# Performance work log

Measured on AMD Instinct MI355X. Metric: run time of the kernel, lower is better.

The kernel has to match this reference:

```python
import jax, jax.numpy as jnp
import numpy as np

B, T, L, D = 4, 64, 4096, 4096
MASK_VALUE = -1000000000.0


def setup_inputs() -> dict:
    key = jax.random.key(0)
    kq, km, ka = jax.random.split(key, 3)
    Q = jax.random.normal(kq, (1, T, D), dtype=jnp.float32)          # learned queries
    mask = jax.random.normal(km, (B, L, D), dtype=jnp.float32)       # acts as K and V
    attn_mask = jax.random.randint(ka, (B, T, L), 0, 2).astype(bool)  # True -> masked
    return {"mask": mask, "Q": Q, "attn_mask": attn_mask}


def reference(mask, Q, attn_mask):
    # scores: [B, T, L] = Q @ mask^T / sqrt(D)   (Q broadcast over batch)
    scale = 1.0 / np.sqrt(D).astype(np.float32)
    scores = jnp.einsum('td,bld->btl', Q[0], mask) * scale
    scores = jnp.where(attn_mask, MASK_VALUE, scores)
    attn = jax.nn.softmax(scores, axis=-1)
    # context: [B, T, D] = attn @ mask
    context = jnp.einsum('btl,bld->btd', attn, mask)
    return context
```

## Files before the change

### kernel.cpp

```cpp
#include <hip/hip_runtime.h>
#include <hip/hip_bf16.h>
#include <stdint.h>

#define B_ 4
#define T_ 64
#define L_ 4096
#define D_ 4096

using bf8   = __attribute__((ext_vector_type(8))) short;
using f32x4 = __attribute__((ext_vector_type(4))) float;

__device__ __forceinline__ unsigned short f2bf(float f) {
    union { float f; unsigned int u; } v;
    v.f = f;
    unsigned int r = v.u + 0x7fffu + ((v.u >> 16) & 1u);
    return (unsigned short)(r >> 16);
}

__device__ __forceinline__ int swz16(int row, int byteoff) {
    return byteoff ^ (((row ^ (row >> 3)) & 7) << 4);
}

__device__ __forceinline__ bf8 read_frag(const unsigned short* lds, int row, int kk, int lane) {
    int byte = kk * 64 + ((lane >> 4) << 4);
    int off  = row * 128 + swz16(row, byte);
    return *reinterpret_cast<const bf8*>(reinterpret_cast<const char*>(lds) + off);
}

__global__ __launch_bounds__(256, 2) void k_scores(
    const float* __restrict__ mask, const float* __restrict__ Q,
    float* __restrict__ scores) {
    __shared__ unsigned short lA[2][64 * 64];
    __shared__ unsigned short lB[2][32 * 64];
    const int tid  = threadIdx.x;
    const int lane = tid & 63;
    const int wave = tid >> 6;
    const int wm = wave >> 1, wn = wave & 1;
    const int b  = blockIdx.y;
    const int l0 = blockIdx.x * 32;
    const float* __restrict__ Mb = mask + (size_t)b * L_ * D_;

    f32x4 acc[2] = {};
    float4 ra[4], rb[2];

    auto loadTiles = [&](int k0) {
#pragma unroll
        for (int s = 0; s < 4; ++s) {
            int slot = tid + s * 256;
            int r = slot >> 4, c4 = slot & 15;
            ra[s] = *(reinterpret_cast<const float4*>(Q + (size_t)r * D_ + k0) + c4);
        }
#pragma unroll
        for (int s = 0; s < 2; ++s) {
            int slot = tid + s * 256;
            int r = slot >> 4, c4 = slot & 15;
            rb[s] = *(reinterpret_cast<const float4*>(Mb + (size_t)(l0 + r) * D_ + k0) + c4);
        }
    };
    auto writeTiles = [&](int buf) {
#pragma unroll
        for (int s = 0; s < 4; ++s) {
            int slot = tid + s * 256;
            int r = slot >> 4, c4 = slot & 15;
            int off = r * 128 + swz16(r, c4 * 8);
            ushort4 ua;
            ua.x = f2bf(ra[s].x); ua.y = f2bf(ra[s].y); ua.z = f2bf(ra[s].z); ua.w = f2bf(ra[s].w);
            *reinterpret_cast<ushort4*>(reinterpret_cast<char*>(lA[buf]) + off) = ua;
        }
#pragma unroll
        for (int s = 0; s < 2; ++s) {
            int slot = tid + s * 256;
            int r = slot >> 4, c4 = slot & 15;
            int off = r * 128 + swz16(r, c4 * 8);
            ushort4 ub;
            ub.x = f2bf(rb[s].x); ub.y = f2bf(rb[s].y); ub.z = f2bf(rb[s].z); ub.w = f2bf(rb[s].w);
            *reinterpret_cast<ushort4*>(reinterpret_cast<char*>(lB[buf]) + off) = ub;
        }
    };

    loadTiles(0);
    writeTiles(0);
    __syncthreads();
    const int NT = D_ / 64;
    for (int kt = 0; kt < NT; ++kt) {
        int cur = kt & 1;
        if (kt + 1 < NT) loadTiles((kt + 1) * 64);
#pragma unroll
        for (int kk = 0; kk < 2; ++kk) {
            bf8 a0 = read_frag(lA[cur], wm * 32 +      (lane & 15), kk, lane);
            bf8 a1 = read_frag(lA[cur], wm * 32 + 16 + (lane & 15), kk, lane);
            bf8 b0 = read_frag(lB[cur], wn * 16 +      (lane & 15), kk, lane);
            acc[0] = __builtin_amdgcn_mfma_f32_16x16x32_bf16(a0, b0, acc[0], 0, 0, 0);
            acc[1] = __builtin_amdgcn_mfma_f32_16x16x32_bf16(a1, b0, acc[1], 0, 0, 0);
        }
        if (kt + 1 < NT) writeTiles(cur ^ 1);
        __syncthreads();
    }

    const int rgrp = (lane >> 4) * 4;
    const int cidx = lane & 15;
#pragma unroll
    for (int mi = 0; mi < 2; ++mi)
#pragma unroll
        for (int r = 0; r < 4; ++r) {
            int t = wm * 32 + mi * 16 + rgrp + r;
            int l = l0 + wn * 16 + cidx;
            scores[((size_t)b * T_ + t) * L_ + l] = acc[mi][r] * 0.015625f;
        }
}

__global__ __launch_bounds__(256, 4) void k_softmax(
    const float* __restrict__ scores, const int* __restrict__ am,
    unsigned short* __restrict__ attn) {
    const int row  = blockIdx.x;
    const int tid  = threadIdx.x;
    const int lane = tid & 63;
    const int wave = tid >> 6;
    const float* __restrict__ s = scores + (size_t)row * L_;
    const int*   __restrict__ m = am     + (size_t)row * L_;
    __shared__ float redmax[4], redsum[4];

    float v[16];
#pragma unroll
    for (int j = 0; j < 4; ++j) {
        float4 f = *(reinterpret_cast<const float4*>(s) + tid + j * 256);
        int4   q = *(reinterpret_cast<const int4*>(m)   + tid + j * 256);
        v[j * 4 + 0] = q.x ? -1.0e9f : f.x;
        v[j * 4 + 1] = q.y ? -1.0e9f : f.y;
        v[j * 4 + 2] = q.z ? -1.0e9f : f.z;
        v[j * 4 + 3] = q.w ? -1.0e9f : f.w;
    }
    float mx = -3.0e38f;
#pragma unroll
    for (int i = 0; i < 16; ++i) mx = fmaxf(mx, v[i]);
#pragma unroll
    for (int off = 32; off; off >>= 1) mx = fmaxf(mx, __shfl_xor(mx, off, 64));
    if (lane == 0) redmax[wave] = mx;
    __syncthreads();
    mx = fmaxf(fmaxf(redmax[0], redmax[1]), fmaxf(redmax[2], redmax[3]));

    float z = 0.f;
#pragma unroll
    for (int i = 0; i < 16; ++i) {
        v[i] = exp2f((v[i] - mx) * 1.4426950408889634f);
        z += v[i];
    }
#pragma unroll
    for (int off = 32; off; off >>= 1) z += __shfl_xor(z, off, 64);
    if (lane == 0) redsum[wave] = z;
    __syncthreads();
    z = (redsum[0] + redsum[1]) + (redsum[2] + redsum[3]);
    float inv = 1.0f / z;

    unsigned short* __restrict__ arow = attn + (size_t)row * L_;
#pragma unroll
    for (int j = 0; j < 4; ++j) {
        ushort4 u;
        u.x = f2bf(v[j * 4 + 0] * inv);
        u.y = f2bf(v[j * 4 + 1] * inv);
        u.z = f2bf(v[j * 4 + 2] * inv);
        u.w = f2bf(v[j * 4 + 3] * inv);
        *(reinterpret_cast<ushort4*>(arow) + tid + j * 256) = u;
    }
}

__global__ __launch_bounds__(256, 2) void k_context(
    const float* __restrict__ mask, const unsigned short* __restrict__ attn,
    float* __restrict__ out) {
    __shared__ unsigned short lA[2][64 * 64];
    __shared__ unsigned short lB[2][32 * 64];
    const int tid  = threadIdx.x;
    const int lane = tid & 63;
    const int wave = tid >> 6;
    const int wm = wave >> 1, wn = wave & 1;
    const int b  = blockIdx.y;
    const int d0 = blockIdx.x * 32;
    const float*          __restrict__ Mb = mask + (size_t)b * L_ * D_;
    const unsigned short* __restrict__ Ab = attn + (size_t)b * T_ * L_;

    f32x4 acc[2] = {};
    uint4  raA[2];
    float4 rbB[2];

    auto loadTiles = [&](int k0) {
#pragma unroll
        for (int s = 0; s < 2; ++s) {
            int slot = tid + s * 256;
            int r = slot >> 3, c8 = slot & 7;
            raA[s] = *(reinterpret_cast<const uint4*>(Ab + (size_t)r * L_ + k0) + c8);
        }
#pragma unroll
        for (int s = 0; s < 2; ++s) {
            int slot = tid + s * 256;
            int kl = slot >> 3, d4 = slot & 7;
            rbB[s] = *(reinterpret_cast<const float4*>(Mb + (size_t)(k0 + kl) * D_ + d0) + d4);
        }
    };
    auto writeTiles = [&](int buf) {
#pragma unroll
        for (int s = 0; s < 2; ++s) {
            int slot = tid + s * 256;
            int r = slot >> 3, c8 = slot & 7;
            int off = r * 128 + swz16(r, c8 * 16);
            *reinterpret_cast<uint4*>(reinterpret_cast<char*>(lA[buf]) + off) = raA[s];
        }
#pragma unroll
        for (int s = 0; s < 2; ++s) {
            int slot = tid + s * 256;
            int kl = slot >> 3, d4 = slot & 7;
            float fv[4] = { rbB[s].x, rbB[s].y, rbB[s].z, rbB[s].w };
#pragma unroll
            for (int i = 0; i < 4; ++i) {
                int d = d4 * 4 + i;
                int off = d * 128 + swz16(d, kl * 2);
                *reinterpret_cast<unsigned short*>(reinterpret_cast<char*>(lB[buf]) + off) = f2bf(fv[i]);
            }
        }
    };

    loadTiles(0);
    writeTiles(0);
    __syncthreads();
    const int NT = L_ / 64;
    for (int kt = 0; kt < NT; ++kt) {
        int cur = kt & 1;
        if (kt + 1 < NT) loadTiles((kt + 1) * 64);
#pragma unroll
        for (int kk = 0; kk < 2; ++kk) {
            bf8 a0 = read_frag(lA[cur], wm * 32 +      (lane & 15), kk, lane);
            bf8 a1 = read_frag(lA[cur], wm * 32 + 16 + (lane & 15), kk, lane);
            bf8 b0 = read_frag(lB[cur], wn * 16 +      (lane & 15), kk, lane);
            acc[0] = __builtin_amdgcn_mfma_f32_16x16x32_bf16(a0, b0, acc[0], 0, 0, 0);
            acc[1] = __builtin_amdgcn_mfma_f32_16x16x32_bf16(a1, b0, acc[1], 0, 0, 0);
        }
        if (kt + 1 < NT) writeTiles(cur ^ 1);
        __syncthreads();
    }

    const int rgrp = (lane >> 4) * 4;
    const int cidx = lane & 15;
#pragma unroll
    for (int mi = 0; mi < 2; ++mi)
#pragma unroll
        for (int r = 0; r < 4; ++r) {
            int t = wm * 32 + mi * 16 + rgrp + r;
            int d = d0 + wn * 16 + cidx;
            out[((size_t)b * T_ + t) * D_ + d] = acc[mi][r];
        }
}

extern "C" void kernel_launch(void* const* d_in, const int* in_sizes, int n_in,
                              void* d_out, int out_size, void* d_ws, size_t ws_size,
                              hipStream_t stream) {
    const float* mask = (const float*)d_in[0];
    const float* Q    = (const float*)d_in[1];
    const int*   am   = (const int*)d_in[2];
    float* out = (float*)d_out;
    unsigned short* attn = (unsigned short*)d_ws;

    k_scores<<<dim3(L_ / 32, B_), 256, 0, stream>>>(mask, Q, out);
    k_softmax<<<dim3(B_ * T_), 256, 0, stream>>>(out, am, attn);
    k_context<<<dim3(D_ / 32, B_), 256, 0, stream>>>(mask, attn, out);
}
```

Before: 139.6 us.

## Replace LDS-staged GEMMs with direct per-wave global-to-MFMA fragment loads

Both GEMM kernels drop the shared-memory double-buffered tiles and barriers. Each wave now loads its MFMA fragments straight from global memory, converting fp32 mask values to bf16 with packed v_cvt_pk_bf16_f32. Q is pre-converted to bf16 by a new small kernel, and scores move to a separate workspace region. The aim is to remove LDS round trips and syncs and raise occupancy. The T dimension is split into two halves handled by different blocks, which can double global reads of the large mask tensor. The context kernel also gathers its B operand with eight strided scalar loads per step.

New measurement: 219.9 us. 1.57x slower.

```diff
diff --git a/kernel.cpp b/kernel.cpp
--- a/kernel.cpp
+++ b/kernel.cpp
@@ -17,96 +17,62 @@
     return (unsigned short)(r >> 16);
 }
 
-__device__ __forceinline__ int swz16(int row, int byteoff) {
-    return byteoff ^ (((row ^ (row >> 3)) & 7) << 4);
+__device__ __forceinline__ unsigned int cvt_pk(float lo, float hi) {
+    unsigned int r;
+    asm("v_cvt_pk_bf16_f32 %0, %1, %2" : "=v"(r) : "v"(lo), "v"(hi));
+    return r;
 }
 
-__device__ __forceinline__ bf8 read_frag(const unsigned short* lds, int row, int kk, int lane) {
-    int byte = kk * 64 + ((lane >> 4) << 4);
-    int off  = row * 128 + swz16(row, byte);
-    return *reinterpret_cast<const bf8*>(reinterpret_cast<const char*>(lds) + off);
+union BF8U { bf8 v; unsigned int u[4]; };
+
+__global__ __launch_bounds__(256) void k_qprep(const float* __restrict__ Q,
+                                               unsigned short* __restrict__ Qbf) {
+    int i = blockIdx.x * 256 + threadIdx.x;
+    float4 f = reinterpret_cast<const float4*>(Q)[i];
+    ushort4 u;
+    u.x = f2bf(f.x); u.y = f2bf(f.y); u.z = f2bf(f.z); u.w = f2bf(f.w);
+    reinterpret_cast<ushort4*>(Qbf)[i] = u;
 }
 
 __global__ __launch_bounds__(256, 2) void k_scores(
-    const float* __restrict__ mask, const float* __restrict__ Q,
+    const float* __restrict__ mask, const unsigned short* __restrict__ Qbf,
     float* __restrict__ scores) {
-    __shared__ unsigned short lA[2][64 * 64];
-    __shared__ unsigned short lB[2][32 * 64];
     const int tid  = threadIdx.x;
     const int lane = tid & 63;
-    const int wave = tid >> 6;
-    const int wm = wave >> 1, wn = wave & 1;
-    const int b  = blockIdx.y;
-    const int l0 = blockIdx.x * 32;
+    const int w    = blockIdx.x * 4 + (tid >> 6);
+    const int lt = w & 255;
+    const int b  = (w >> 8) & 3;
+    const int th = w >> 10;
+    const int l0 = lt * 16, t0 = th * 32;
+    const int lr = lane & 15, hi = lane >> 4;
+
     const float* __restrict__ Mb = mask + (size_t)b * L_ * D_;
+    const float* __restrict__ pB = Mb + (size_t)(l0 + lr) * D_ + hi * 8;
+    const unsigned short* __restrict__ pA0 = Qbf + (size_t)(t0 + lr) * D_ + hi * 8;
+    const unsigned short* __restrict__ pA1 = pA0 + 16 * D_;
 
-    f32x4 acc[2] = {};
-    float4 ra[4], rb[2];
-
-    auto loadTiles = [&](int k0) {
-#pragma unroll
-        for (int s = 0; s < 4; ++s) {
-            int slot = tid + s * 256;
-            int r = slot >> 4, c4 = slot & 15;
-            ra[s] = *(reinterpret_cast<const float4*>(Q + (size_t)r * D_ + k0) + c4);
-        }
-#pragma unroll
-        for (int s = 0; s < 2; ++s) {
-            int slot = tid + s * 256;
-            int r = slot >> 4, c4 = slot & 15;
-            rb[s] = *(reinterpret_cast<const float4*>(Mb + (size_t)(l0 + r) * D_ + k0) + c4);
-        }
-    };
-    auto writeTiles = [&](int buf) {
-#pragma unroll
-        for (int s = 0; s < 4; ++s) {
-            int slot = tid + s * 256;
-            int r = slot >> 4, c4 = slot & 15;
-            int off = r * 128 + swz16(r, c4 * 8);
-            ushort4 ua;
-            ua.x = f2bf(ra[s].x); ua.y = f2bf(ra[s].y); ua.z = f2bf(ra[s].z); ua.w = f2bf(ra[s].w);
-            *reinterpret_cast<ushort4*>(reinterpret_cast<char*>(lA[buf]) + off) = ua;
-        }
-#pragma unroll
-        for (int s = 0; s < 2; ++s) {
-            int slot = tid + s * 256;
-            int r = slot >> 4, c4 = slot & 15;
-            int off = r * 128 + swz16(r, c4 * 8);
-            ushort4 ub;
-            ub.x = f2bf(rb[s].x); ub.y = f2bf(rb[s].y); ub.z = f2bf(rb[s].z); ub.w = f2bf(rb[s].w);
-            *reinterpret_cast<ushort4*>(reinterpret_cast<char*>(lB[buf]) + off) = ub;
-        }
-    };
-
-    loadTiles(0);
-    writeTiles(0);
-    __syncthreads();
-    const int NT = D_ / 64;
-    for (int kt = 0; kt < NT; ++kt) {
-        int cur = kt & 1;
-        if (kt + 1 < NT) loadTiles((kt + 1) * 64);
-#pragma unroll
-        for (int kk = 0; kk < 2; ++kk) {
-            bf8 a0 = read_frag(lA[cur], wm * 32 +      (lane & 15), kk, lane);
-            bf8 a1 = read_frag(lA[cur], wm * 32 + 16 + (lane & 15), kk, lane);
-            bf8 b0 = read_frag(lB[cur], wn * 16 +      (lane & 15), kk, lane);
-            acc[0] = __builtin_amdgcn_mfma_f32_16x16x32_bf16(a0, b0, acc[0], 0, 0, 0);
-            acc[1] = __builtin_amdgcn_mfma_f32_16x16x32_bf16(a1, b0, acc[1], 0, 0, 0);
-        }
-        if (kt + 1 < NT) writeTiles(cur ^ 1);
-        __syncthreads();
+    f32x4 acc0 = {}, acc1 = {};
+#pragma unroll 4
+    for (int k0 = 0; k0 < D_; k0 += 32) {
+        float4 f0 = *reinterpret_cast<const float4*>(pB + k0);
+        float4 f1 = *reinterpret_cast<const float4*>(pB + k0 + 4);
+        bf8 a0 = *reinterpret_cast<const bf8*>(pA0 + k0);
+        bf8 a1 = *reinterpret_cast<const bf8*>(pA1 + k0);
+        BF8U bb;
+        bb.u[0] = cvt_pk(f0.x, f0.y);
+        bb.u[1] = cvt_pk(f0.z, f0.w);
+        bb.u[2] = cvt_pk(f1.x, f1.y);
+        bb.u[3] = cvt_pk(f1.z, f1.w);
+        acc0 = __builtin_amdgcn_mfma_f32_16x16x32_bf16(a0, bb.v, acc0, 0, 0, 0);
+        acc1 = __builtin_amdgcn_mfma_f32_16x16x32_bf16(a1, bb.v, acc1, 0, 0, 0);
     }
 
-    const int rgrp = (lane >> 4) * 4;
-    const int cidx = lane & 15;
+    float* __restrict__ srow = scores + ((size_t)b * T_ + t0) * L_ + l0 + lr;
 #pragma unroll
-    for (int mi = 0; mi < 2; ++mi)
-#pragma unroll
-        for (int r = 0; r < 4; ++r) {
-            int t = wm * 32 + mi * 16 + rgrp + r;
-            int l = l0 + wn * 16 + cidx;
-            scores[((size_t)b * T_ + t) * L_ + l] = acc[mi][r] * 0.015625f;
-        }
+    for (int r = 0; r < 4; ++r) {
+        srow[(size_t)(hi * 4 + r) * L_]        = acc0[r] * 0.015625f;
+        srow[(size_t)(16 + hi * 4 + r) * L_]   = acc1[r] * 0.015625f;
+    }
 }
 
 __global__ __launch_bounds__(256, 4) void k_softmax(
@@ -167,86 +133,44 @@
 __global__ __launch_bounds__(256, 2) void k_context(
     const float* __restrict__ mask, const unsigned short* __restrict__ attn,
     float* __restrict__ out) {
-    __shared__ unsigned short lA[2][64 * 64];
-    __shared__ unsigned short lB[2][32 * 64];
     const int tid  = threadIdx.x;
     const int lane = tid & 63;
-    const int wave = tid >> 6;
-    const int wm = wave >> 1, wn = wave & 1;
-    const int b  = blockIdx.y;
-    const int d0 = blockIdx.x * 32;
+    const int w    = blockIdx.x * 4 + (tid >> 6);
+    const int dt = w & 255;
+    const int b  = (w >> 8) & 3;
+    const int th = w >> 10;
+    const int d0 = dt * 16, t0 = th * 32;
+    const int lr = lane & 15, hi = lane >> 4;
+
     const float*          __restrict__ Mb = mask + (size_t)b * L_ * D_;
     const unsigned short* __restrict__ Ab = attn + (size_t)b * T_ * L_;
+    const unsigned short* __restrict__ pA0 = Ab + (size_t)(t0 + lr) * L_ + hi * 8;
+    const unsigned short* __restrict__ pA1 = pA0 + 16 * L_;
+    const float* __restrict__ pB = Mb + (size_t)(hi * 8) * D_ + d0 + lr;
 
-    f32x4 acc[2] = {};
-    uint4  raA[2];
-    float4 rbB[2];
-
-    auto loadTiles = [&](int k0) {
-#pragma unroll
-        for (int s = 0; s < 2; ++s) {
-            int slot = tid + s * 256;
-            int r = slot >> 3, c8 = slot & 7;
-            raA[s] = *(reinterpret_cast<const uint4*>(Ab + (size_t)r * L_ + k0) + c8);
-        }
-#pragma unroll
-        for (int s = 0; s < 2; ++s) {
-            int slot = tid + s * 256;
-            int kl = slot >> 3, d4 = slot & 7;
-            rbB[s] = *(reinterpret_cast<const float4*>(Mb + (size_t)(k0 + kl) * D_ + d0) + d4);
-        }
-    };
-    auto writeTiles = [&](int buf) {
-#pragma unroll
-        for (int s = 0; s < 2; ++s) {
-            int slot = tid + s * 256;
-            int r = slot >> 3, c8 = slot & 7;
-            int off = r * 128 + swz16(r, c8 * 16);
-            *reinterpret_cast<uint4*>(reinterpret_cast<char*>(lA[buf]) + off) = raA[s];
-        }
-#pragma unroll
-        for (int s = 0; s < 2; ++s) {
-            int slot = tid + s * 256;
-            int kl = slot >> 3, d4 = slot & 7;
-            float fv[4] = { rbB[s].x, rbB[s].y, rbB[s].z, rbB[s].w };
-#pragma unroll
-            for (int i = 0; i < 4; ++i) {
-                int d = d4 * 4 + i;
-                int off = d * 128 + swz16(d, kl * 2);
-                *reinterpret_cast<unsigned short*>(reinterpret_cast<char*>(lB[buf]) + off) = f2bf(fv[i]);
-            }
-        }
-    };
-
-    loadTiles(0);
-    writeTiles(0);
-    __syncthreads();
-    const int NT = L_ / 64;
-    for (int kt = 0; kt < NT; ++kt) {
-        int cur = kt & 1;
-        if (kt + 1 < NT) loadTiles((kt + 1) * 64);
-#pragma unroll
-        for (int kk = 0; kk < 2; ++kk) {
-            bf8 a0 = read_frag(lA[cur], wm * 32 +      (lane & 15), kk, lane);
-            bf8 a1 = read_frag(lA[cur], wm * 32 + 16 + (lane & 15), kk, lane);
-            bf8 b0 = read_frag(lB[cur], wn * 16 +      (lane & 15), kk, lane);
-            acc[0] = __builtin_amdgcn_mfma_f32_16x16x32_bf16(a0, b0, acc[0], 0, 0, 0);
-            acc[1] = __builtin_amdgcn_mfma_f32_16x16x32_bf16(a1, b0, acc[1], 0, 0, 0);
-        }
-        if (kt + 1 < NT) writeTiles(cur ^ 1);
-        __syncthreads();
+    f32x4 acc0 = {}, acc1 = {};
+#pragma unroll 2
+    for (int k0 = 0; k0 < L_; k0 += 32) {
+        const float* __restrict__ pb = pB + (size_t)k0 * D_;
+        float b0 = pb[0 * D_], b1 = pb[1 * D_], b2 = pb[2 * D_], b3 = pb[3 * D_];
+        float b4 = pb[4 * D_], b5 = pb[5 * D_], b6 = pb[6 * D_], b7 = pb[7 * D_];
+        bf8 a0 = *reinterpret_cast<const bf8*>(pA0 + k0);
+        bf8 a1 = *reinterpret_cast<const bf8*>(pA1 + k0);
+        BF8U bb;
+        bb.u[0] = cvt_pk(b0, b1);
+        bb.u[1] = cvt_pk(b2, b3);
+        bb.u[2] = cvt_pk(b4, b5);
+        bb.u[3] = cvt_pk(b6, b7);
+        acc0 = __builtin_amdgcn_mfma_f32_16x16x32_bf16(a0, bb.v, acc0, 0, 0, 0);
+        acc1 = __builtin_amdgcn_mfma_f32_16x16x32_bf16(a1, bb.v, acc1, 0, 0, 0);
     }
 
-    const int rgrp = (lane >> 4) * 4;
-    const int cidx = lane & 15;
+    float* __restrict__ orow = out + ((size_t)b * T_ + t0) * D_ + d0 + lr;
 #pragma unroll
-    for (int mi = 0; mi < 2; ++mi)
-#pragma unroll
-        for (int r = 0; r < 4; ++r) {
-            int t = wm * 32 + mi * 16 + rgrp + r;
-            int d = d0 + wn * 16 + cidx;
-            out[((size_t)b * T_ + t) * D_ + d] = acc[mi][r];
-        }
+    for (int r = 0; r < 4; ++r) {
+        orow[(size_t)(hi * 4 + r) * D_]      = acc0[r];
+        orow[(size_t)(16 + hi * 4 + r) * D_] = acc1[r];
+    }
 }
 
 extern "C" void kernel_launch(void* const* d_in, const int* in_sizes, int n_in,
@@ -256,9 +180,13 @@
     const float* Q    = (const float*)d_in[1];
     const int*   am   = (const int*)d_in[2];
     float* out = (float*)d_out;
+
     unsigned short* attn = (unsigned short*)d_ws;
+    unsigned short* Qbf  = (unsigned short*)((char*)d_ws + (2u << 20));
+    float*          scrs = (float*)((char*)d_ws + (2u << 20) + (512u << 10));
 
-    k_scores<<<dim3(L_ / 32, B_), 256, 0, stream>>>(mask, Q, out);
-    k_softmax<<<dim3(B_ * T_), 256, 0, stream>>>(out, am, attn);
-    k_context<<<dim3(D_ / 32, B_), 256, 0, stream>>>(mask, attn, out);
+    k_qprep<<<dim3(T_ * D_ / 4 / 256), 256, 0, stream>>>(Q, Qbf);
+    k_scores<<<dim3(512), 256, 0, stream>>>(mask, Qbf, scrs);
+    k_softmax<<<dim3(B_ * T_), 256, 0, stream>>>(scrs, am, attn);
+    k_context<<<dim3(512), 256, 0, stream>>>(mask, attn, out);
 }
```
